# Optimization experiments

Hardware: AMD Instinct MI355X
Metric: run time of the kernel (lower is better)

The kernel has to match this reference:

```python
import jax, jax.numpy as jnp
import numpy as np

# MACE layer restricted to l_max=1 (irreps 0e+1o), correlation=3, selector_tp=False,
# last_layer=False, soft_normalization=None, 1 readout head.
N = 50000      # nodes
E = 400000     # edges
C = 64         # channels (multiplicity)
S = 10         # species
R = 8          # radial basis size
AVG = 8.0      # avg_num_neighbors


def setup_inputs() -> dict:
    key = jax.random.key(0)
    ks = jax.random.split(key, 20)
    inp = {}
    inp["edge_vectors"] = jax.random.normal(ks[0], (E, 3), jnp.float32)
    inp["node_feats"] = jax.random.normal(ks[1], (N, C, 4), jnp.float32)  # [:, :, 0]=0e, [:, :, 1:]=1o
    inp["node_species"] = jax.random.randint(ks[2], (N,), 0, S)
    inp["radial_embeddings"] = jax.random.normal(ks[3], (E, R), jnp.float32)
    inp["senders"] = jax.random.randint(ks[4], (E,), 0, N)
    inp["receivers"] = jax.random.randint(ks[5], (E,), 0, N)
    # radial MLP -> per-path, per-channel tensor-product weights (4 CG paths for (0e+1o)x(0e+1o)->0e+1o)
    inp["W_r1"] = jax.random.normal(ks[6], (R, 64), jnp.float32) / np.float32(np.sqrt(R))
    inp["W_r2"] = jax.random.normal(ks[7], (64, 64), jnp.float32) / 8.0
    inp["W_r3"] = jax.random.normal(ks[8], (64, 4 * C), jnp.float32) / 8.0
    # linear (per-irrep channel mixing) after message aggregation
    inp["W_lin0"] = jax.random.normal(ks[9], (C, C), jnp.float32) / 8.0
    inp["W_lin1"] = jax.random.normal(ks[10], (C, C), jnp.float32) / 8.0
    # symmetric contraction weights (per species), correlation up to 3
    inp["Wsc0"] = jax.random.normal(ks[11], (S, C, 5), jnp.float32) * 0.1
    inp["Wsc1"] = jax.random.normal(ks[12], (S, C, 4), jnp.float32) * 0.1
    # linear after product basis block
    inp["Wp0"] = jax.random.normal(ks[13], (C, C), jnp.float32) / 8.0
    inp["Wp1"] = jax.random.normal(ks[14], (C, C), jnp.float32) / 8.0
    # residual FullyConnectedTensorProduct(node_feats, species one-hot) == species-conditioned linear
    inp["Wres0"] = jax.random.normal(ks[15], (S, C, C), jnp.float32) / 8.0
    inp["Wres1"] = jax.random.normal(ks[16], (S, C, C), jnp.float32) / 8.0
    # linear readout: 0e channels -> scalar output
    inp["W_read"] = jax.random.normal(ks[17], (C, 1), jnp.float32) / 8.0
    return inp


def reference(edge_vectors, node_feats, node_species, radial_embeddings, senders, receivers,
              W_r1, W_r2, W_r3, W_lin0, W_lin1, Wsc0, Wsc1, Wp0, Wp1, Wres0, Wres1, W_read):
    onehot = jax.nn.one_hot(node_species, S, dtype=node_feats.dtype)  # [N, S]
    x0 = node_feats[:, :, 0]      # [N, C] scalars
    x1 = node_feats[:, :, 1:]     # [N, C, 3] vectors

    # --- residual connection: FCTP with species one-hot (species-dependent channel mixing) ---
    res0 = jnp.einsum('ns,scd,nc->nd', onehot, Wres0, x0)
    res1 = jnp.einsum('ns,scd,nci->ndi', onehot, Wres1, x1)

    # --- InteractionBlock ---
    # spherical harmonics l=1 with component normalization
    r = jnp.sqrt(jnp.sum(edge_vectors * edge_vectors, axis=-1, keepdims=True) + 1e-12)
    Y1 = jnp.sqrt(jnp.asarray(3.0, edge_vectors.dtype)) * edge_vectors / r  # [E, 3]
    # radial MLP -> TP path weights [E, 4, C]
    h = jax.nn.silu(radial_embeddings @ W_r1)
    h = jax.nn.silu(h @ W_r2)
    w = (h @ W_r3).reshape(radial_embeddings.shape[0], 4, C)
    xs0 = x0[senders]             # [E, C]
    xs1 = x1[senders]             # [E, C, 3]
    # CG tensor product paths: 0e out: (0e x Y0), (1o . Y1); 1o out: (0e * Y1), (1o * Y0)
    m0 = w[:, 0] * xs0 + w[:, 1] * jnp.einsum('eci,ei->ec', xs1, Y1)            # [E, C]
    m1 = (w[:, 2] * xs0)[:, :, None] * Y1[:, None, :] + w[:, 3][:, :, None] * xs1  # [E, C, 3]
    a0 = jax.ops.segment_sum(m0, receivers, num_segments=N) / AVG
    a1 = jax.ops.segment_sum(m1, receivers, num_segments=N) / AVG
    A0 = a0 @ W_lin0
    A1 = jnp.einsum('nci,cd->ndi', a1, W_lin1)

    # --- EquivariantProductBasisBlock: symmetric contraction, correlation 3, per-species weights ---
    w0 = jnp.einsum('ns,scp->ncp', onehot, Wsc0)  # [N, C, 5]
    w1 = jnp.einsum('ns,scp->ncp', onehot, Wsc1)  # [N, C, 4]
    n1 = jnp.sum(A1 * A1, axis=-1)                # [N, C] invariant |A1|^2
    B0 = (w0[..., 0] * A0 + w0[..., 1] * A0 * A0 + w0[..., 2] * A0 * A0 * A0
          + w0[..., 3] * n1 + w0[..., 4] * A0 * n1)
    B1 = (w1[..., 0] + w1[..., 1] * A0 + w1[..., 2] * A0 * A0 + w1[..., 3] * n1)[..., None] * A1
    F0 = B0 @ Wp0 + res0
    F1 = jnp.einsum('nci,cd->ndi', B1, Wp1) + res1

    node_feats_out = jnp.concatenate([F0[..., None], F1], axis=-1)  # [N, C, 4]
    node_outputs = (F0 @ W_read)[:, None, :]                         # [N, heads=1, 1]
    return node_outputs, node_feats_out
```

## Files before the change

### kernel.cpp

```cpp
#include <hip/hip_runtime.h>


typedef __attribute__((ext_vector_type(8))) short bf16x8;
typedef __attribute__((ext_vector_type(4))) float f32x4;

constexpr int kN = 50000;
constexpr int kE = 400000;
constexpr int kS = 10;
constexpr int kTilesMax = 3150;

constexpr size_t kOffM    = 0;
constexpr size_t kOffCnt  = 204800000;
constexpr size_t kOffCnt2 = 205000000;
constexpr size_t kOffOff  = 205000064;
constexpr size_t kOffOff2 = 205200128;
constexpr size_t kOffCur  = 205200192;
constexpr size_t kOffCur2 = 205400192;
constexpr size_t kOffPos  = 205400256;
constexpr size_t kOffNidx = 207000256;
constexpr size_t kOffWlT0 = 207201856;
constexpr size_t kOffWlT1 = 207210048;
constexpr size_t kOffWpT0 = 207218240;
constexpr size_t kOffWpT1 = 207226432;
constexpr size_t kOffWrT0 = 207234624;
constexpr size_t kOffWrT1 = 207316544;

__device__ __forceinline__ float silu_f(float x) {
    float t = __expf(-x);
    return x / (1.0f + t);
}
__device__ __forceinline__ unsigned short f2bf(float f) {
    unsigned u = __float_as_uint(f);
    unsigned r = (u + 0x7FFFu + ((u >> 16) & 1u)) >> 16;
    return (unsigned short)r;
}
__device__ __forceinline__ float bf2f(unsigned short b) {
    return __uint_as_float(((unsigned)b) << 16);
}
__device__ __forceinline__ int swz128(int row, int byteoff) {
    return row * 128 + (byteoff ^ ((row & 7) << 4));
}

__global__ __launch_bounds__(256)
void prep_kernel(const int* __restrict__ rcv, const int* __restrict__ spc,
                 const float* __restrict__ Wl0, const float* __restrict__ Wl1,
                 const float* __restrict__ Wp0, const float* __restrict__ Wp1,
                 const float* __restrict__ Wres0, const float* __restrict__ Wres1,
                 int* __restrict__ cnt, int* __restrict__ cnt2,
                 unsigned short* __restrict__ WlT0, unsigned short* __restrict__ WlT1,
                 unsigned short* __restrict__ WpT0, unsigned short* __restrict__ WpT1,
                 unsigned short* __restrict__ WrT0, unsigned short* __restrict__ WrT1)
{
    const int tid = threadIdx.x;
    const int gtid = blockIdx.x * 256 + tid;
    const int gstride = gridDim.x * 256;

    for (int i = gtid; i < kE; i += gstride) atomicAdd(&cnt[rcv[i]], 1);

    __shared__ int lh[kS];
    for (int base = blockIdx.x * 256; base < kN; base += gstride) {
        if (tid < kS) lh[tid] = 0;
        __syncthreads();
        int node = base + tid;
        if (node < kN) atomicAdd(&lh[spc[node]], 1);
        __syncthreads();
        if (tid < kS && lh[tid]) atomicAdd(&cnt2[tid], lh[tid]);
        __syncthreads();
    }

    for (int i3 = gtid; i3 < 16384 + 81920; i3 += gstride) {
        if (i3 < 16384) {
            int w = i3 >> 12, r = i3 & 4095, k = r >> 6, n = r & 63;
            const float* src = (w == 0) ? Wl0 : (w == 1) ? Wl1 : (w == 2) ? Wp0 : Wp1;
            unsigned short* dst = (w == 0) ? WlT0 : (w == 1) ? WlT1 : (w == 2) ? WpT0 : WpT1;
            dst[swz128(n, 2 * k) >> 1] = f2bf(src[r]);
        } else {
            int i4 = i3 - 16384;
            int w = i4 / 40960;
            int r5 = i4 - w * 40960;
            int s = r5 >> 12, r = r5 & 4095, k = r >> 6, n = r & 63;
            const float* src = w ? Wres1 : Wres0;
            unsigned short* dst = w ? WrT1 : WrT0;
            dst[(s << 12) + (swz128(n, 2 * k) >> 1)] = f2bf(src[r5]);
        }
    }
}

__global__ __launch_bounds__(1024)
void scan_kernel(const int* __restrict__ cnt, int* __restrict__ off,
                 int* __restrict__ cur,
                 const int* __restrict__ cnt2, int* __restrict__ off2,
                 int* __restrict__ cur2)
{
    __shared__ int wred[16];
    const int tid = threadIdx.x;
    const int lane = tid & 63;
    const int wv = tid >> 6;
    const int CH = 49;
    const int b = tid * CH;
    int s = 0;
    for (int i = 0; i < CH; ++i) {
        int idx = b + i;
        if (idx < kN) s += cnt[idx];
    }
    int incl = s;
    for (int d = 1; d < 64; d <<= 1) {
        int t = __shfl_up(incl, d, 64);
        if (lane >= d) incl += t;
    }
    if (lane == 63) wred[wv] = incl;
    __syncthreads();
    if (tid < 16) {
        int o = wred[tid];
        int v = o;
        for (int d = 1; d < 16; d <<= 1) {
            int t = __shfl_up(v, d, 64);
            if (tid >= d) v += t;
        }
        wred[tid] = v - o;
    }
    __syncthreads();
    int run = wred[wv] + (incl - s);
    for (int i = 0; i < CH; ++i) {
        int idx = b + i;
        if (idx < kN) {
            int c = cnt[idx];
            off[idx] = run;
            cur[idx] = run;
            run += c;
        }
    }
    if (tid == 0) {
        off[kN] = kE;
        int base = 0;
        for (int sp = 0; sp < kS; ++sp) {
            off2[sp] = base;
            cur2[sp] = base;
            base += (cnt2[sp] + 15) & ~15;
        }
        off2[kS] = base;
    }
}

__global__ __launch_bounds__(256)
void rank_kernel(const int* __restrict__ rcv, const int* __restrict__ spc,
                 int* __restrict__ cur, int* __restrict__ pos,
                 int* __restrict__ cur2, int* __restrict__ nidx)
{
    const int tid = threadIdx.x;
    const int gstride = gridDim.x * 256;

    for (int i = blockIdx.x * 256 + tid; i < kE; i += gstride)
        pos[i] = atomicAdd(&cur[rcv[i]], 1);

    __shared__ int lh[kS];
    __shared__ int gbase[kS];
    for (int base = blockIdx.x * 256; base < kN; base += gstride) {
        if (tid < kS) lh[tid] = 0;
        __syncthreads();
        const int node = base + tid;
        int s = -1, lr = 0;
        if (node < kN) {
            s = spc[node];
            lr = atomicAdd(&lh[s], 1);
        }
        __syncthreads();
        if (tid < kS) gbase[tid] = lh[tid] ? atomicAdd(&cur2[tid], lh[tid]) : 0;
        __syncthreads();
        if (node < kN) nidx[gbase[s] + lr] = node;
        __syncthreads();
    }
}

__global__ __launch_bounds__(512, 1)
void edge_mfma(const float* __restrict__ ev,
               const float* __restrict__ nf,
               const float* __restrict__ rad,
               const int* __restrict__ snd,
               const int* __restrict__ pos,
               const float* __restrict__ W1,
               const float* __restrict__ W2,
               const float* __restrict__ W3,
               unsigned short* __restrict__ mq)
{
    __shared__ unsigned short W2T[64 * 64];
    __shared__ unsigned short W3T[256 * 64];
    __shared__ unsigned short h1s[8][16 * 64];
    __shared__ unsigned short h2s[8][16 * 64];
    __shared__ unsigned short wTs[8][256 * 20];

    const int tid = threadIdx.x;
    for (int i = tid; i < 64 * 64; i += 512) {
        int k = i >> 6, n = i & 63;
        W2T[swz128(n, 2 * k) >> 1] = f2bf(W2[i]);
    }
    for (int i = tid; i < 256 * 64; i += 512) {
        int k = i >> 8, n = i & 255;
        W3T[swz128(n, 2 * k) >> 1] = f2bf(W3[i]);
    }
    __syncthreads();

    const int lane = tid & 63;
    const int wvi = tid >> 6;
    const int l15 = lane & 15;
    const int g = lane >> 4;

    float w1r[8];
#pragma unroll
    for (int r = 0; r < 8; ++r) w1r[r] = W1[(r << 6) | lane];

    unsigned short* h1w = h1s[wvi];
    unsigned short* h2w = h2s[wvi];
    unsigned short* wTw = wTs[wvi];

    for (int t = blockIdx.x; t < kE / 128; t += gridDim.x) {
        const int et = t * 128 + wvi * 16;

        for (int e = 0; e < 16; ++e) {
            const float4 ra = *(const float4*)&rad[(size_t)(et + e) * 8];
            const float4 rb = *(const float4*)&rad[(size_t)(et + e) * 8 + 4];
            float acc = ra.x * w1r[0] + ra.y * w1r[1] + ra.z * w1r[2] + ra.w * w1r[3]
                      + rb.x * w1r[4] + rb.y * w1r[5] + rb.z * w1r[6] + rb.w * w1r[7];
            h1w[swz128(e, 2 * lane) >> 1] = f2bf(silu_f(acc));
        }
        __builtin_amdgcn_wave_barrier();

        bf16x8 a0 = *(const bf16x8*)&h1w[swz128(l15, g * 16) >> 1];
        bf16x8 a1 = *(const bf16x8*)&h1w[swz128(l15, 64 + g * 16) >> 1];

#pragma unroll
        for (int n0 = 0; n0 < 64; n0 += 16) {
            const int n = n0 + l15;
            bf16x8 b0 = *(const bf16x8*)&W2T[swz128(n, g * 16) >> 1];
            bf16x8 b1 = *(const bf16x8*)&W2T[swz128(n, 64 + g * 16) >> 1];
            f32x4 acc = {0.f, 0.f, 0.f, 0.f};
            acc = __builtin_amdgcn_mfma_f32_16x16x32_bf16(a0, b0, acc, 0, 0, 0);
            acc = __builtin_amdgcn_mfma_f32_16x16x32_bf16(a1, b1, acc, 0, 0, 0);
#pragma unroll
            for (int r = 0; r < 4; ++r) {
                int e2 = g * 4 + r;
                h2w[swz128(e2, 2 * n) >> 1] = f2bf(silu_f(acc[r]));
            }
        }
        __builtin_amdgcn_wave_barrier();

        bf16x8 c0 = *(const bf16x8*)&h2w[swz128(l15, g * 16) >> 1];
        bf16x8 c1 = *(const bf16x8*)&h2w[swz128(l15, 64 + g * 16) >> 1];
#pragma unroll
        for (int m0 = 0; m0 < 16; ++m0) {
            const int nrow = m0 * 16 + l15;
            bf16x8 wa0 = *(const bf16x8*)&W3T[swz128(nrow, g * 16) >> 1];
            bf16x8 wa1 = *(const bf16x8*)&W3T[swz128(nrow, 64 + g * 16) >> 1];
            f32x4 acc = {0.f, 0.f, 0.f, 0.f};
            acc = __builtin_amdgcn_mfma_f32_16x16x32_bf16(wa0, c0, acc, 0, 0, 0);
            acc = __builtin_amdgcn_mfma_f32_16x16x32_bf16(wa1, c1, acc, 0, 0, 0);
#pragma unroll
            for (int r = 0; r < 4; ++r) {
                int nn = m0 * 16 + g * 4 + r;
                wTw[nn * 20 + l15] = f2bf(acc[r]);
            }
        }
        __builtin_amdgcn_wave_barrier();

        const int c = lane;
#pragma unroll
        for (int grp = 0; grp < 4; ++grp) {
            ushort4 qa[4];
#pragma unroll
            for (int k = 0; k < 4; ++k)
                qa[k] = *(const ushort4*)&wTw[(k * 64 + c) * 20 + grp * 4];
            const unsigned short* qp = (const unsigned short*)qa;
#pragma unroll
            for (int e = 0; e < 4; ++e) {
                const int eid = et + grp * 4 + e;
                const int sid = snd[eid];
                const int p = pos[eid];
                const float ex = ev[(size_t)eid * 3 + 0];
                const float ey = ev[(size_t)eid * 3 + 1];
                const float ez = ev[(size_t)eid * 3 + 2];
                const float ri = rsqrtf(ex * ex + ey * ey + ez * ez + 1e-12f);
                const float y0 = 1.7320508075688772f * ex * ri;
                const float y1 = 1.7320508075688772f * ey * ri;
                const float y2 = 1.7320508075688772f * ez * ri;
                const float4 xv = *(const float4*)&nf[(((size_t)sid << 6) | c) << 2];
                const float w0 = bf2f(qp[0 * 4 + e]);
                const float w1 = bf2f(qp[1 * 4 + e]);
                const float w2v = bf2f(qp[2 * 4 + e]);
                const float w3v = bf2f(qp[3 * 4 + e]);
                const float dot1 = xv.y * y0 + xv.z * y1 + xv.w * y2;
                const float m0v = w0 * xv.x + w1 * dot1;
                const float t2 = w2v * xv.x;
                ushort4 q;
                q.x = f2bf(m0v);
                q.y = f2bf(t2 * y0 + w3v * xv.y);
                q.z = f2bf(t2 * y1 + w3v * xv.z);
                q.w = f2bf(t2 * y2 + w3v * xv.w);
                *(ushort4*)&mq[((size_t)p << 8) + (c << 2)] = q;
            }
        }
        __builtin_amdgcn_wave_barrier();
    }
}

__global__ __launch_bounds__(256, 2)
void node_mfma(const float* __restrict__ nf, const int* __restrict__ spc,
               const unsigned short* __restrict__ WlT0, const unsigned short* __restrict__ WlT1,
               const unsigned short* __restrict__ WpT0, const unsigned short* __restrict__ WpT1,
               const unsigned short* __restrict__ WrT0, const unsigned short* __restrict__ WrT1,
               const float* __restrict__ Wsc0, const float* __restrict__ Wsc1,
               const float* __restrict__ Wrd,
               const unsigned short* __restrict__ m, const int* __restrict__ off,
               const int* __restrict__ nidx,
               float* __restrict__ out0, float* __restrict__ outF)
{
    __shared__ unsigned short slab[8][1024];
    __shared__ float roS[4][16];

    const int tid = threadIdx.x;
    const int lane = tid & 63;
    const int wvi = tid >> 6;
    const int l15 = lane & 15;
    const int g = lane >> 4;
    const int tb = (int)blockIdx.x << 4;

    const int c = lane;
    for (int e4 = 0; e4 < 4; ++e4) {
        const int e = wvi * 4 + e4;
        const int node = nidx[tb + e];
        float ax = 0.f, ay = 0.f, az = 0.f, aw = 0.f;
        if (node >= 0) {
            const int beg = off[node], end = off[node + 1];
            for (int i = beg; i < end; ++i) {
                const ushort4 q = *(const ushort4*)&m[((size_t)i << 8) + (c << 2)];
                ax += bf2f(q.x); ay += bf2f(q.y); az += bf2f(q.z); aw += bf2f(q.w);
            }
        }
        const float vv[4] = {ax * 0.125f, ay * 0.125f, az * 0.125f, aw * 0.125f};
        const int o = swz128(e, 2 * c) >> 1;
#pragma unroll
        for (int p = 0; p < 4; ++p) {
            const unsigned short hi = f2bf(vv[p]);
            slab[p][o] = hi;
            slab[4 + p][o] = f2bf(vv[p] - bf2f(hi));
        }
    }
    __syncthreads();

    const int n0 = nidx[tb];
    if (n0 < 0) return;
    const int s = spc[n0];

    bf16x8 aF[8][2];
#pragma unroll
    for (int p = 0; p < 8; ++p) {
        aF[p][0] = *(const bf16x8*)&slab[p][swz128(l15, g * 16) >> 1];
        aF[p][1] = *(const bf16x8*)&slab[p][swz128(l15, 64 + g * 16) >> 1];
    }
    __syncthreads();

    const int d = l15 + 16 * wvi;
    {
        bf16x8 bl0a = *(const bf16x8*)&WlT0[swz128(d, g * 16) >> 1];
        bf16x8 bl0b = *(const bf16x8*)&WlT0[swz128(d, 64 + g * 16) >> 1];
        bf16x8 bl1a = *(const bf16x8*)&WlT1[swz128(d, g * 16) >> 1];
        bf16x8 bl1b = *(const bf16x8*)&WlT1[swz128(d, 64 + g * 16) >> 1];
        f32x4 A0v = {0.f, 0.f, 0.f, 0.f};
        f32x4 Axv = {0.f, 0.f, 0.f, 0.f};
        f32x4 Ayv = {0.f, 0.f, 0.f, 0.f};
        f32x4 Azv = {0.f, 0.f, 0.f, 0.f};
        A0v = __builtin_amdgcn_mfma_f32_16x16x32_bf16(aF[0][0], bl0a, A0v, 0, 0, 0);
        A0v = __builtin_amdgcn_mfma_f32_16x16x32_bf16(aF[0][1], bl0b, A0v, 0, 0, 0);
        A0v = __builtin_amdgcn_mfma_f32_16x16x32_bf16(aF[4][0], bl0a, A0v, 0, 0, 0);
        A0v = __builtin_amdgcn_mfma_f32_16x16x32_bf16(aF[4][1], bl0b, A0v, 0, 0, 0);
        Axv = __builtin_amdgcn_mfma_f32_16x16x32_bf16(aF[1][0], bl1a, Axv, 0, 0, 0);
        Axv = __builtin_amdgcn_mfma_f32_16x16x32_bf16(aF[1][1], bl1b, Axv, 0, 0, 0);
        Axv = __builtin_amdgcn_mfma_f32_16x16x32_bf16(aF[5][0], bl1a, Axv, 0, 0, 0);
        Axv = __builtin_amdgcn_mfma_f32_16x16x32_bf16(aF[5][1], bl1b, Axv, 0, 0, 0);
        Ayv = __builtin_amdgcn_mfma_f32_16x16x32_bf16(aF[2][0], bl1a, Ayv, 0, 0, 0);
        Ayv = __builtin_amdgcn_mfma_f32_16x16x32_bf16(aF[2][1], bl1b, Ayv, 0, 0, 0);
        Ayv = __builtin_amdgcn_mfma_f32_16x16x32_bf16(aF[6][0], bl1a, Ayv, 0, 0, 0);
        Ayv = __builtin_amdgcn_mfma_f32_16x16x32_bf16(aF[6][1], bl1b, Ayv, 0, 0, 0);
        Azv = __builtin_amdgcn_mfma_f32_16x16x32_bf16(aF[3][0], bl1a, Azv, 0, 0, 0);
        Azv = __builtin_amdgcn_mfma_f32_16x16x32_bf16(aF[3][1], bl1b, Azv, 0, 0, 0);
        Azv = __builtin_amdgcn_mfma_f32_16x16x32_bf16(aF[7][0], bl1a, Azv, 0, 0, 0);
        Azv = __builtin_amdgcn_mfma_f32_16x16x32_bf16(aF[7][1], bl1b, Azv, 0, 0, 0);

        const float* w0p = &Wsc0[((s << 6) | d) * 5];
        const float c0 = w0p[0], c1 = w0p[1], c2 = w0p[2], c3 = w0p[3], c4 = w0p[4];
        const float4 w1v = *(const float4*)&Wsc1[((s << 6) | d) << 2];

#pragma unroll
        for (int r = 0; r < 4; ++r) {
            const float A0 = A0v[r], Ax = Axv[r], Ay = Ayv[r], Az = Azv[r];
            const float n1 = Ax * Ax + Ay * Ay + Az * Az;
            const float A0sq = A0 * A0;
            const float B0 = c0 * A0 + c1 * A0sq + c2 * A0sq * A0 + c3 * n1 + c4 * A0 * n1;
            const float gg = w1v.x + w1v.y * A0 + w1v.z * A0sq + w1v.w * n1;
            const float bb[4] = {B0, gg * Ax, gg * Ay, gg * Az};
            const int o = swz128(g * 4 + r, 2 * d) >> 1;
#pragma unroll
            for (int p = 0; p < 4; ++p) {
                const unsigned short hi = f2bf(bb[p]);
                slab[p][o] = hi;
                slab[4 + p][o] = f2bf(bb[p] - bf2f(hi));
            }
        }
    }
    __syncthreads();

    bf16x8 bF[8][2];
#pragma unroll
    for (int p = 0; p < 8; ++p) {
        bF[p][0] = *(const bf16x8*)&slab[p][swz128(l15, g * 16) >> 1];
        bF[p][1] = *(const bf16x8*)&slab[p][swz128(l15, 64 + g * 16) >> 1];
    }
    const int xnode = nidx[tb + l15];
    bf16x8 xF[4][2];
#pragma unroll
    for (int h = 0; h < 2; ++h) {
#pragma unroll
        for (int j = 0; j < 8; ++j) {
            const int k = h * 32 + g * 8 + j;
            float4 v = make_float4(0.f, 0.f, 0.f, 0.f);
            if (xnode >= 0) v = *(const float4*)&nf[(((size_t)xnode << 6) | k) << 2];
            xF[0][h][j] = (short)f2bf(v.x);
            xF[1][h][j] = (short)f2bf(v.y);
            xF[2][h][j] = (short)f2bf(v.z);
            xF[3][h][j] = (short)f2bf(v.w);
        }
    }

    const int ndr0 = nidx[tb + g * 4 + 0];
    const int ndr1 = nidx[tb + g * 4 + 1];
    const int ndr2 = nidx[tb + g * 4 + 2];
    const int ndr3 = nidx[tb + g * 4 + 3];

    {
        bf16x8 bp0a = *(const bf16x8*)&WpT0[swz128(d, g * 16) >> 1];
        bf16x8 bp0b = *(const bf16x8*)&WpT0[swz128(d, 64 + g * 16) >> 1];
        bf16x8 bp1a = *(const bf16x8*)&WpT1[swz128(d, g * 16) >> 1];
        bf16x8 bp1b = *(const bf16x8*)&WpT1[swz128(d, 64 + g * 16) >> 1];
        const unsigned short* wr0 = &WrT0[(size_t)s << 12];
        const unsigned short* wr1 = &WrT1[(size_t)s << 12];
        bf16x8 br0a = *(const bf16x8*)&wr0[swz128(d, g * 16) >> 1];
        bf16x8 br0b = *(const bf16x8*)&wr0[swz128(d, 64 + g * 16) >> 1];
        bf16x8 br1a = *(const bf16x8*)&wr1[swz128(d, g * 16) >> 1];
        bf16x8 br1b = *(const bf16x8*)&wr1[swz128(d, 64 + g * 16) >> 1];

        f32x4 F0v = {0.f, 0.f, 0.f, 0.f};
        f32x4 Fxv = {0.f, 0.f, 0.f, 0.f};
        f32x4 Fyv = {0.f, 0.f, 0.f, 0.f};
        f32x4 Fzv = {0.f, 0.f, 0.f, 0.f};
        F0v = __builtin_amdgcn_mfma_f32_16x16x32_bf16(bF[0][0], bp0a, F0v, 0, 0, 0);
        F0v = __builtin_amdgcn_mfma_f32_16x16x32_bf16(bF[0][1], bp0b, F0v, 0, 0, 0);
        F0v = __builtin_amdgcn_mfma_f32_16x16x32_bf16(bF[4][0], bp0a, F0v, 0, 0, 0);
        F0v = __builtin_amdgcn_mfma_f32_16x16x32_bf16(bF[4][1], bp0b, F0v, 0, 0, 0);
        F0v = __builtin_amdgcn_mfma_f32_16x16x32_bf16(xF[0][0], br0a, F0v, 0, 0, 0);
        F0v = __builtin_amdgcn_mfma_f32_16x16x32_bf16(xF[0][1], br0b, F0v, 0, 0, 0);
        Fxv = __builtin_amdgcn_mfma_f32_16x16x32_bf16(bF[1][0], bp1a, Fxv, 0, 0, 0);
        Fxv = __builtin_amdgcn_mfma_f32_16x16x32_bf16(bF[1][1], bp1b, Fxv, 0, 0, 0);
        Fxv = __builtin_amdgcn_mfma_f32_16x16x32_bf16(bF[5][0], bp1a, Fxv, 0, 0, 0);
        Fxv = __builtin_amdgcn_mfma_f32_16x16x32_bf16(bF[5][1], bp1b, Fxv, 0, 0, 0);
        Fxv = __builtin_amdgcn_mfma_f32_16x16x32_bf16(xF[1][0], br1a, Fxv, 0, 0, 0);
        Fxv = __builtin_amdgcn_mfma_f32_16x16x32_bf16(xF[1][1], br1b, Fxv, 0, 0, 0);
        Fyv = __builtin_amdgcn_mfma_f32_16x16x32_bf16(bF[2][0], bp1a, Fyv, 0, 0, 0);
        Fyv = __builtin_amdgcn_mfma_f32_16x16x32_bf16(bF[2][1], bp1b, Fyv, 0, 0, 0);
        Fyv = __builtin_amdgcn_mfma_f32_16x16x32_bf16(bF[6][0], bp1a, Fyv, 0, 0, 0);
        Fyv = __builtin_amdgcn_mfma_f32_16x16x32_bf16(bF[6][1], bp1b, Fyv, 0, 0, 0);
        Fyv = __builtin_amdgcn_mfma_f32_16x16x32_bf16(xF[2][0], br1a, Fyv, 0, 0, 0);
        Fyv = __builtin_amdgcn_mfma_f32_16x16x32_bf16(xF[2][1], br1b, Fyv, 0, 0, 0);
        Fzv = __builtin_amdgcn_mfma_f32_16x16x32_bf16(bF[3][0], bp1a, Fzv, 0, 0, 0);
        Fzv = __builtin_amdgcn_mfma_f32_16x16x32_bf16(bF[3][1], bp1b, Fzv, 0, 0, 0);
        Fzv = __builtin_amdgcn_mfma_f32_16x16x32_bf16(bF[7][0], bp1a, Fzv, 0, 0, 0);
        Fzv = __builtin_amdgcn_mfma_f32_16x16x32_bf16(bF[7][1], bp1b, Fzv, 0, 0, 0);
        Fzv = __builtin_amdgcn_mfma_f32_16x16x32_bf16(xF[3][0], br1a, Fzv, 0, 0, 0);
        Fzv = __builtin_amdgcn_mfma_f32_16x16x32_bf16(xF[3][1], br1b, Fzv, 0, 0, 0);

        const float wdv = Wrd[d];
        if (ndr0 >= 0) *(float4*)&outF[((size_t)ndr0 << 8) + (d << 2)] = make_float4(F0v[0], Fxv[0], Fyv[0], Fzv[0]);
        if (ndr1 >= 0) *(float4*)&outF[((size_t)ndr1 << 8) + (d << 2)] = make_float4(F0v[1], Fxv[1], Fyv[1], Fzv[1]);
        if (ndr2 >= 0) *(float4*)&outF[((size_t)ndr2 << 8) + (d << 2)] = make_float4(F0v[2], Fxv[2], Fyv[2], Fzv[2]);
        if (ndr3 >= 0) *(float4*)&outF[((size_t)ndr3 << 8) + (d << 2)] = make_float4(F0v[3], Fxv[3], Fyv[3], Fzv[3]);

        float ro[4] = {F0v[0] * wdv, F0v[1] * wdv, F0v[2] * wdv, F0v[3] * wdv};
#pragma unroll
        for (int mo = 1; mo < 16; mo <<= 1) {
#pragma unroll
            for (int r = 0; r < 4; ++r) ro[r] += __shfl_xor(ro[r], mo, 64);
        }
        if (l15 == 0) {
#pragma unroll
            for (int r = 0; r < 4; ++r) roS[wvi][g * 4 + r] = ro[r];
        }
    }
    __syncthreads();

    if (tid < 16) {
        const int nd = nidx[tb + tid];
        if (nd >= 0)
            out0[nd] = roS[0][tid] + roS[1][tid] + roS[2][tid] + roS[3][tid];
    }
}

extern "C" void kernel_launch(void* const* d_in, const int* in_sizes, int n_in,
                              void* d_out, int out_size, void* d_ws, size_t ws_size,
                              hipStream_t stream)
{
    const float* edge_vectors = (const float*)d_in[0];
    const float* node_feats   = (const float*)d_in[1];
    const int*   node_species = (const int*)d_in[2];
    const float* radial       = (const float*)d_in[3];
    const int*   senders      = (const int*)d_in[4];
    const int*   receivers    = (const int*)d_in[5];
    const float* W_r1   = (const float*)d_in[6];
    const float* W_r2   = (const float*)d_in[7];
    const float* W_r3   = (const float*)d_in[8];
    const float* W_lin0 = (const float*)d_in[9];
    const float* W_lin1 = (const float*)d_in[10];
    const float* Wsc0   = (const float*)d_in[11];
    const float* Wsc1   = (const float*)d_in[12];
    const float* Wp0    = (const float*)d_in[13];
    const float* Wp1    = (const float*)d_in[14];
    const float* Wres0  = (const float*)d_in[15];
    const float* Wres1  = (const float*)d_in[16];
    const float* W_read = (const float*)d_in[17];

    float* out0 = (float*)d_out;
    float* outF = out0 + kN;

    char* ws = (char*)d_ws;
    unsigned short* m = (unsigned short*)(ws + kOffM);
    int* cnt  = (int*)(ws + kOffCnt);
    int* cnt2 = (int*)(ws + kOffCnt2);
    int* off  = (int*)(ws + kOffOff);
    int* off2 = (int*)(ws + kOffOff2);
    int* cur  = (int*)(ws + kOffCur);
    int* cur2 = (int*)(ws + kOffCur2);
    int* pos  = (int*)(ws + kOffPos);
    int* nidx = (int*)(ws + kOffNidx);
    unsigned short* WlT0 = (unsigned short*)(ws + kOffWlT0);
    unsigned short* WlT1 = (unsigned short*)(ws + kOffWlT1);
    unsigned short* WpT0 = (unsigned short*)(ws + kOffWpT0);
    unsigned short* WpT1 = (unsigned short*)(ws + kOffWpT1);
    unsigned short* WrT0 = (unsigned short*)(ws + kOffWrT0);
    unsigned short* WrT1 = (unsigned short*)(ws + kOffWrT1);

    hipMemsetAsync(cnt, 0, kN * sizeof(int) + 64, stream);
    hipMemsetAsync(nidx, 0xFF, (size_t)kTilesMax * 16 * sizeof(int), stream);

    prep_kernel<<<1024, 256, 0, stream>>>(receivers, node_species,
                                          W_lin0, W_lin1, Wp0, Wp1, Wres0, Wres1,
                                          cnt, cnt2,
                                          WlT0, WlT1, WpT0, WpT1, WrT0, WrT1);
    scan_kernel<<<1, 1024, 0, stream>>>(cnt, off, cur, cnt2, off2, cur2);
    rank_kernel<<<1024, 256, 0, stream>>>(receivers, node_species,
                                          cur, pos, cur2, nidx);

    edge_mfma<<<256, 512, 0, stream>>>(edge_vectors, node_feats, radial,
                                       senders, pos, W_r1, W_r2, W_r3, m);

    node_mfma<<<kTilesMax, 256, 0, stream>>>(
        node_feats, node_species,
        WlT0, WlT1, WpT0, WpT1, WrT0, WrT1,
        Wsc0, Wsc1, W_read,
        m, off, nidx, out0, outF);
}
```

Measured before the change: 459.8 us.

## Fuse edge ranking into counting, MFMA first radial layer, drop LDS transpose

Edge ranks now come from the atomic counting pass in prep_kernel, and the scan adds the offset later, so the second atomic pass over edges goes away. In edge_mfma the first radial layer runs as an MFMA, and the per-channel TP weights stay in registers instead of going through an LDS transpose. Each lane handles one edge, with 512 blocks and a higher occupancy hint. Other changes: a hardware packed bf16 conversion, and a 4-way unrolled segment sum in the node kernel. The risks are higher register pressure from keeping 16 accumulators live, and more scattered nf gathers.

Result: no change. 457.7 us (-0.5%).

```diff
diff --git a/kernel.cpp b/kernel.cpp
--- a/kernel.cpp
+++ b/kernel.cpp
@@ -29,10 +29,13 @@
     float t = __expf(-x);
     return x / (1.0f + t);
 }
-__device__ __forceinline__ unsigned short f2bf(float f) {
-    unsigned u = __float_as_uint(f);
-    unsigned r = (u + 0x7FFFu + ((u >> 16) & 1u)) >> 16;
-    return (unsigned short)r;
+__device__ __forceinline__ unsigned cvt_pk_bf16(float lo, float hi) {
+    unsigned r;
+    asm("v_cvt_pk_bf16_f32 %0, %1, %2" : "=v"(r) : "v"(lo), "v"(hi));
+    return r;
+}
+__device__ __forceinline__ unsigned short f2bf1(float x) {
+    return (unsigned short)cvt_pk_bf16(x, 0.f);
 }
 __device__ __forceinline__ float bf2f(unsigned short b) {
     return __uint_as_float(((unsigned)b) << 16);
@@ -47,6 +50,7 @@
                  const float* __restrict__ Wp0, const float* __restrict__ Wp1,
                  const float* __restrict__ Wres0, const float* __restrict__ Wres1,
                  int* __restrict__ cnt, int* __restrict__ cnt2,
+                 int* __restrict__ pos,
                  unsigned short* __restrict__ WlT0, unsigned short* __restrict__ WlT1,
                  unsigned short* __restrict__ WpT0, unsigned short* __restrict__ WpT1,
                  unsigned short* __restrict__ WrT0, unsigned short* __restrict__ WrT1)
@@ -55,7 +59,7 @@
     const int gtid = blockIdx.x * 256 + tid;
     const int gstride = gridDim.x * 256;
 
-    for (int i = gtid; i < kE; i += gstride) atomicAdd(&cnt[rcv[i]], 1);
+    for (int i = gtid; i < kE; i += gstride) pos[i] = atomicAdd(&cnt[rcv[i]], 1);
 
     __shared__ int lh[kS];
     for (int base = blockIdx.x * 256; base < kN; base += gstride) {
@@ -73,7 +77,7 @@
             int w = i3 >> 12, r = i3 & 4095, k = r >> 6, n = r & 63;
             const float* src = (w == 0) ? Wl0 : (w == 1) ? Wl1 : (w == 2) ? Wp0 : Wp1;
             unsigned short* dst = (w == 0) ? WlT0 : (w == 1) ? WlT1 : (w == 2) ? WpT0 : WpT1;
-            dst[swz128(n, 2 * k) >> 1] = f2bf(src[r]);
+            dst[swz128(n, 2 * k) >> 1] = f2bf1(src[r]);
         } else {
             int i4 = i3 - 16384;
             int w = i4 / 40960;
@@ -81,14 +85,13 @@
             int s = r5 >> 12, r = r5 & 4095, k = r >> 6, n = r & 63;
             const float* src = w ? Wres1 : Wres0;
             unsigned short* dst = w ? WrT1 : WrT0;
-            dst[(s << 12) + (swz128(n, 2 * k) >> 1)] = f2bf(src[r5]);
+            dst[(s << 12) + (swz128(n, 2 * k) >> 1)] = f2bf1(src[r5]);
         }
     }
 }
 
 __global__ __launch_bounds__(1024)
 void scan_kernel(const int* __restrict__ cnt, int* __restrict__ off,
-                 int* __restrict__ cur,
                  const int* __restrict__ cnt2, int* __restrict__ off2,
                  int* __restrict__ cur2)
 {
@@ -124,10 +127,8 @@
     for (int i = 0; i < CH; ++i) {
         int idx = b + i;
         if (idx < kN) {
-            int c = cnt[idx];
             off[idx] = run;
-            cur[idx] = run;
-            run += c;
+            run += cnt[idx];
         }
     }
     if (tid == 0) {
@@ -143,40 +144,33 @@
 }
 
 __global__ __launch_bounds__(256)
-void rank_kernel(const int* __restrict__ rcv, const int* __restrict__ spc,
-                 int* __restrict__ cur, int* __restrict__ pos,
-                 int* __restrict__ cur2, int* __restrict__ nidx)
+void noderank_kernel(const int* __restrict__ spc,
+                     int* __restrict__ cur2, int* __restrict__ nidx)
 {
-    const int tid = threadIdx.x;
-    const int gstride = gridDim.x * 256;
-
-    for (int i = blockIdx.x * 256 + tid; i < kE; i += gstride)
-        pos[i] = atomicAdd(&cur[rcv[i]], 1);
-
     __shared__ int lh[kS];
     __shared__ int gbase[kS];
-    for (int base = blockIdx.x * 256; base < kN; base += gstride) {
-        if (tid < kS) lh[tid] = 0;
-        __syncthreads();
-        const int node = base + tid;
-        int s = -1, lr = 0;
-        if (node < kN) {
-            s = spc[node];
-            lr = atomicAdd(&lh[s], 1);
-        }
-        __syncthreads();
-        if (tid < kS) gbase[tid] = lh[tid] ? atomicAdd(&cur2[tid], lh[tid]) : 0;
-        __syncthreads();
-        if (node < kN) nidx[gbase[s] + lr] = node;
-        __syncthreads();
-    }
-}
-
-__global__ __launch_bounds__(512, 1)
+    const int tid = threadIdx.x;
+    const int node = blockIdx.x * 256 + tid;
+    if (tid < kS) lh[tid] = 0;
+    __syncthreads();
+    int s = -1, lr = 0;
+    if (node < kN) {
+        s = spc[node];
+        lr = atomicAdd(&lh[s], 1);
+    }
+    __syncthreads();
+    if (tid < kS) gbase[tid] = lh[tid] ? atomicAdd(&cur2[tid], lh[tid]) : 0;
+    __syncthreads();
+    if (node < kN) nidx[gbase[s] + lr] = node;
+}
+
+__global__ __launch_bounds__(512, 4)
 void edge_mfma(const float* __restrict__ ev,
                const float* __restrict__ nf,
                const float* __restrict__ rad,
                const int* __restrict__ snd,
+               const int* __restrict__ rcv,
+               const int* __restrict__ off,
                const int* __restrict__ pos,
                const float* __restrict__ W1,
                const float* __restrict__ W2,
@@ -187,16 +181,15 @@
     __shared__ unsigned short W3T[256 * 64];
     __shared__ unsigned short h1s[8][16 * 64];
     __shared__ unsigned short h2s[8][16 * 64];
-    __shared__ unsigned short wTs[8][256 * 20];
 
     const int tid = threadIdx.x;
     for (int i = tid; i < 64 * 64; i += 512) {
         int k = i >> 6, n = i & 63;
-        W2T[swz128(n, 2 * k) >> 1] = f2bf(W2[i]);
+        W2T[swz128(n, 2 * k) >> 1] = f2bf1(W2[i]);
     }
     for (int i = tid; i < 256 * 64; i += 512) {
         int k = i >> 8, n = i & 255;
-        W3T[swz128(n, 2 * k) >> 1] = f2bf(W3[i]);
+        W3T[swz128(n, 2 * k) >> 1] = f2bf1(W3[i]);
     }
     __syncthreads();
 
@@ -205,29 +198,57 @@
     const int l15 = lane & 15;
     const int g = lane >> 4;
 
-    float w1r[8];
-#pragma unroll
-    for (int r = 0; r < 8; ++r) w1r[r] = W1[(r << 6) | lane];
+    bf16x8 w1f[4];
+#pragma unroll
+    for (int t4 = 0; t4 < 4; ++t4) {
+        union { unsigned u[4]; bf16x8 v; } t;
+        if (g == 0) {
+            const int n = t4 * 16 + l15;
+            float a[8];
+#pragma unroll
+            for (int j = 0; j < 8; ++j) a[j] = W1[j * 64 + n];
+            t.u[0] = cvt_pk_bf16(a[0], a[1]);
+            t.u[1] = cvt_pk_bf16(a[2], a[3]);
+            t.u[2] = cvt_pk_bf16(a[4], a[5]);
+            t.u[3] = cvt_pk_bf16(a[6], a[7]);
+        } else {
+            t.u[0] = t.u[1] = t.u[2] = t.u[3] = 0u;
+        }
+        w1f[t4] = t.v;
+    }
 
     unsigned short* h1w = h1s[wvi];
     unsigned short* h2w = h2s[wvi];
-    unsigned short* wTw = wTs[wvi];
 
     for (int t = blockIdx.x; t < kE / 128; t += gridDim.x) {
         const int et = t * 128 + wvi * 16;
 
-        for (int e = 0; e < 16; ++e) {
-            const float4 ra = *(const float4*)&rad[(size_t)(et + e) * 8];
-            const float4 rb = *(const float4*)&rad[(size_t)(et + e) * 8 + 4];
-            float acc = ra.x * w1r[0] + ra.y * w1r[1] + ra.z * w1r[2] + ra.w * w1r[3]
-                      + rb.x * w1r[4] + rb.y * w1r[5] + rb.z * w1r[6] + rb.w * w1r[7];
-            h1w[swz128(e, 2 * lane) >> 1] = f2bf(silu_f(acc));
+        union { unsigned u[4]; bf16x8 v; } tr;
+        if (g == 0) {
+            const float4 ra = *(const float4*)&rad[(size_t)(et + l15) * 8];
+            const float4 rb = *(const float4*)&rad[(size_t)(et + l15) * 8 + 4];
+            tr.u[0] = cvt_pk_bf16(ra.x, ra.y);
+            tr.u[1] = cvt_pk_bf16(ra.z, ra.w);
+            tr.u[2] = cvt_pk_bf16(rb.x, rb.y);
+            tr.u[3] = cvt_pk_bf16(rb.z, rb.w);
+        } else {
+            tr.u[0] = tr.u[1] = tr.u[2] = tr.u[3] = 0u;
+        }
+        const bf16x8 aR = tr.v;
+
+#pragma unroll
+        for (int t4 = 0; t4 < 4; ++t4) {
+            f32x4 acc = {0.f, 0.f, 0.f, 0.f};
+            acc = __builtin_amdgcn_mfma_f32_16x16x32_bf16(aR, w1f[t4], acc, 0, 0, 0);
+            const int n = t4 * 16 + l15;
+#pragma unroll
+            for (int r = 0; r < 4; ++r)
+                h1w[swz128(g * 4 + r, 2 * n) >> 1] = f2bf1(silu_f(acc[r]));
         }
         __builtin_amdgcn_wave_barrier();
 
         bf16x8 a0 = *(const bf16x8*)&h1w[swz128(l15, g * 16) >> 1];
         bf16x8 a1 = *(const bf16x8*)&h1w[swz128(l15, 64 + g * 16) >> 1];
-
 #pragma unroll
         for (int n0 = 0; n0 < 64; n0 += 16) {
             const int n = n0 + l15;
@@ -237,65 +258,53 @@
             acc = __builtin_amdgcn_mfma_f32_16x16x32_bf16(a0, b0, acc, 0, 0, 0);
             acc = __builtin_amdgcn_mfma_f32_16x16x32_bf16(a1, b1, acc, 0, 0, 0);
 #pragma unroll
-            for (int r = 0; r < 4; ++r) {
-                int e2 = g * 4 + r;
-                h2w[swz128(e2, 2 * n) >> 1] = f2bf(silu_f(acc[r]));
-            }
+            for (int r = 0; r < 4; ++r)
+                h2w[swz128(g * 4 + r, 2 * n) >> 1] = f2bf1(silu_f(acc[r]));
         }
         __builtin_amdgcn_wave_barrier();
+
+        const int eid = et + l15;
+        const int sid = snd[eid];
+        const int p = off[rcv[eid]] + pos[eid];
+        const float ex = ev[(size_t)eid * 3 + 0];
+        const float ey = ev[(size_t)eid * 3 + 1];
+        const float ez = ev[(size_t)eid * 3 + 2];
+        const float ri = rsqrtf(ex * ex + ey * ey + ez * ez + 1e-12f);
+        const float y0 = 1.7320508075688772f * ex * ri;
+        const float y1 = 1.7320508075688772f * ey * ri;
+        const float y2 = 1.7320508075688772f * ez * ri;
 
         bf16x8 c0 = *(const bf16x8*)&h2w[swz128(l15, g * 16) >> 1];
         bf16x8 c1 = *(const bf16x8*)&h2w[swz128(l15, 64 + g * 16) >> 1];
+        f32x4 acc[16];
 #pragma unroll
         for (int m0 = 0; m0 < 16; ++m0) {
             const int nrow = m0 * 16 + l15;
             bf16x8 wa0 = *(const bf16x8*)&W3T[swz128(nrow, g * 16) >> 1];
             bf16x8 wa1 = *(const bf16x8*)&W3T[swz128(nrow, 64 + g * 16) >> 1];
-            f32x4 acc = {0.f, 0.f, 0.f, 0.f};
-            acc = __builtin_amdgcn_mfma_f32_16x16x32_bf16(wa0, c0, acc, 0, 0, 0);
-            acc = __builtin_amdgcn_mfma_f32_16x16x32_bf16(wa1, c1, acc, 0, 0, 0);
-#pragma unroll
-            for (int r = 0; r < 4; ++r) {
-                int nn = m0 * 16 + g * 4 + r;
-                wTw[nn * 20 + l15] = f2bf(acc[r]);
-            }
-        }
-        __builtin_amdgcn_wave_barrier();
-
-        const int c = lane;
-#pragma unroll
-        for (int grp = 0; grp < 4; ++grp) {
-            ushort4 qa[4];
-#pragma unroll
-            for (int k = 0; k < 4; ++k)
-                qa[k] = *(const ushort4*)&wTw[(k * 64 + c) * 20 + grp * 4];
-            const unsigned short* qp = (const unsigned short*)qa;
-#pragma unroll
-            for (int e = 0; e < 4; ++e) {
-                const int eid = et + grp * 4 + e;
-                const int sid = snd[eid];
-                const int p = pos[eid];
-                const float ex = ev[(size_t)eid * 3 + 0];
-                const float ey = ev[(size_t)eid * 3 + 1];
-                const float ez = ev[(size_t)eid * 3 + 2];
-                const float ri = rsqrtf(ex * ex + ey * ey + ez * ez + 1e-12f);
-                const float y0 = 1.7320508075688772f * ex * ri;
-                const float y1 = 1.7320508075688772f * ey * ri;
-                const float y2 = 1.7320508075688772f * ez * ri;
-                const float4 xv = *(const float4*)&nf[(((size_t)sid << 6) | c) << 2];
-                const float w0 = bf2f(qp[0 * 4 + e]);
-                const float w1 = bf2f(qp[1 * 4 + e]);
-                const float w2v = bf2f(qp[2 * 4 + e]);
-                const float w3v = bf2f(qp[3 * 4 + e]);
+            f32x4 a = {0.f, 0.f, 0.f, 0.f};
+            a = __builtin_amdgcn_mfma_f32_16x16x32_bf16(wa0, c0, a, 0, 0, 0);
+            a = __builtin_amdgcn_mfma_f32_16x16x32_bf16(wa1, c1, a, 0, 0, 0);
+            acc[m0] = a;
+        }
+
+#pragma unroll
+        for (int hi = 0; hi < 4; ++hi) {
+#pragma unroll
+            for (int lo = 0; lo < 4; ++lo) {
+                const int c = hi * 16 + g * 4 + lo;
+                const float4 xv = *(const float4*)&nf[((size_t)sid << 8) + (c << 2)];
+                const float w0 = acc[hi][lo];
+                const float w1 = acc[4 + hi][lo];
+                const float w2v = acc[8 + hi][lo];
+                const float w3v = acc[12 + hi][lo];
                 const float dot1 = xv.y * y0 + xv.z * y1 + xv.w * y2;
                 const float m0v = w0 * xv.x + w1 * dot1;
                 const float t2 = w2v * xv.x;
-                ushort4 q;
-                q.x = f2bf(m0v);
-                q.y = f2bf(t2 * y0 + w3v * xv.y);
-                q.z = f2bf(t2 * y1 + w3v * xv.z);
-                q.w = f2bf(t2 * y2 + w3v * xv.w);
-                *(ushort4*)&mq[((size_t)p << 8) + (c << 2)] = q;
+                const unsigned q01 = cvt_pk_bf16(m0v, t2 * y0 + w3v * xv.y);
+                const unsigned q23 = cvt_pk_bf16(t2 * y1 + w3v * xv.z,
+                                                 t2 * y2 + w3v * xv.w);
+                *(uint2*)&mq[(size_t)p * 256 + (c << 2)] = make_uint2(q01, q23);
             }
         }
         __builtin_amdgcn_wave_barrier();
@@ -330,7 +339,18 @@
         float ax = 0.f, ay = 0.f, az = 0.f, aw = 0.f;
         if (node >= 0) {
             const int beg = off[node], end = off[node + 1];
-            for (int i = beg; i < end; ++i) {
+            int i = beg;
+            for (; i + 4 <= end; i += 4) {
+                const ushort4 q0 = *(const ushort4*)&m[((size_t)(i + 0) << 8) + (c << 2)];
+                const ushort4 q1 = *(const ushort4*)&m[((size_t)(i + 1) << 8) + (c << 2)];
+                const ushort4 q2 = *(const ushort4*)&m[((size_t)(i + 2) << 8) + (c << 2)];
+                const ushort4 q3 = *(const ushort4*)&m[((size_t)(i + 3) << 8) + (c << 2)];
+                ax += (bf2f(q0.x) + bf2f(q1.x)) + (bf2f(q2.x) + bf2f(q3.x));
+                ay += (bf2f(q0.y) + bf2f(q1.y)) + (bf2f(q2.y) + bf2f(q3.y));
+                az += (bf2f(q0.z) + bf2f(q1.z)) + (bf2f(q2.z) + bf2f(q3.z));
+                aw += (bf2f(q0.w) + bf2f(q1.w)) + (bf2f(q2.w) + bf2f(q3.w));
+            }
+            for (; i < end; ++i) {
                 const ushort4 q = *(const ushort4*)&m[((size_t)i << 8) + (c << 2)];
                 ax += bf2f(q.x); ay += bf2f(q.y); az += bf2f(q.z); aw += bf2f(q.w);
             }
@@ -339,9 +359,9 @@
         const int o = swz128(e, 2 * c) >> 1;
 #pragma unroll
         for (int p = 0; p < 4; ++p) {
-            const unsigned short hi = f2bf(vv[p]);
+            const unsigned short hi = f2bf1(vv[p]);
             slab[p][o] = hi;
-            slab[4 + p][o] = f2bf(vv[p] - bf2f(hi));
+            slab[4 + p][o] = f2bf1(vv[p] - bf2f(hi));
         }
     }
     __syncthreads();
@@ -400,9 +420,9 @@
             const int o = swz128(g * 4 + r, 2 * d) >> 1;
 #pragma unroll
             for (int p = 0; p < 4; ++p) {
-                const unsigned short hi = f2bf(bb[p]);
+                const unsigned short hi = f2bf1(bb[p]);
                 slab[p][o] = hi;
-                slab[4 + p][o] = f2bf(bb[p] - bf2f(hi));
+                slab[4 + p][o] = f2bf1(bb[p] - bf2f(hi));
             }
         }
     }
@@ -423,10 +443,10 @@
             const int k = h * 32 + g * 8 + j;
             float4 v = make_float4(0.f, 0.f, 0.f, 0.f);
             if (xnode >= 0) v = *(const float4*)&nf[(((size_t)xnode << 6) | k) << 2];
-            xF[0][h][j] = (short)f2bf(v.x);
-            xF[1][h][j] = (short)f2bf(v.y);
-            xF[2][h][j] = (short)f2bf(v.z);
-            xF[3][h][j] = (short)f2bf(v.w);
+            xF[0][h][j] = (short)f2bf1(v.x);
+            xF[1][h][j] = (short)f2bf1(v.y);
+            xF[2][h][j] = (short)f2bf1(v.z);
+            xF[3][h][j] = (short)f2bf1(v.w);
         }
     }
 
@@ -534,7 +554,6 @@
     int* cnt2 = (int*)(ws + kOffCnt2);
     int* off  = (int*)(ws + kOffOff);
     int* off2 = (int*)(ws + kOffOff2);
-    int* cur  = (int*)(ws + kOffCur);
     int* cur2 = (int*)(ws + kOffCur2);
     int* pos  = (int*)(ws + kOffPos);
     int* nidx = (int*)(ws + kOffNidx);
@@ -550,14 +569,14 @@
 
     prep_kernel<<<1024, 256, 0, stream>>>(receivers, node_species,
                                           W_lin0, W_lin1, Wp0, Wp1, Wres0, Wres1,
-                                          cnt, cnt2,
+                                          cnt, cnt2, pos,
                                           WlT0, WlT1, WpT0, WpT1, WrT0, WrT1);
-    scan_kernel<<<1, 1024, 0, stream>>>(cnt, off, cur, cnt2, off2, cur2);
-    rank_kernel<<<1024, 256, 0, stream>>>(receivers, node_species,
-                                          cur, pos, cur2, nidx);
-
-    edge_mfma<<<256, 512, 0, stream>>>(edge_vectors, node_feats, radial,
-                                       senders, pos, W_r1, W_r2, W_r3, m);
+    scan_kernel<<<1, 1024, 0, stream>>>(cnt, off, cnt2, off2, cur2);
+    noderank_kernel<<<(kN + 255) / 256, 256, 0, stream>>>(node_species, cur2, nidx);
+
+    edge_mfma<<<512, 512, 0, stream>>>(edge_vectors, node_feats, radial,
+                                       senders, receivers, off, pos,
+                                       W_r1, W_r2, W_r3, m);
 
     node_mfma<<<kTilesMax, 256, 0, stream>>>(
         node_feats, node_species,
```
